# Kernel optimization log

Hardware: AMD Instinct MI355X
Metric: run time of the kernel (lower is better)

Reference implementation:

```python
import jax, jax.numpy as jnp
import numpy as np

FLT_BACKWARP = 2.5  # Matching.fltBackwarp for intLevel == 4
NEG_SLOPE = 0.1


def backwarp(ten_input, ten_flow):
    # torch grid_sample(mode='bilinear', padding_mode='zeros', align_corners=True)
    # with grid = base + flow*2/(size-1) is equivalent to sampling at pixel coords
    # (x + u, y + v) with zero padding outside [0, W-1] x [0, H-1].
    B, C, H, W = ten_input.shape
    xs = jnp.arange(W, dtype=ten_input.dtype)
    ys = jnp.arange(H, dtype=ten_input.dtype)
    px = xs[None, None, :] + ten_flow[:, 0]  # [B,H,W]
    py = ys[None, :, None] + ten_flow[:, 1]  # [B,H,W]
    x0 = jnp.floor(px)
    y0 = jnp.floor(py)
    x1 = x0 + 1.0
    y1 = y0 + 1.0
    wx1 = px - x0
    wx0 = 1.0 - wx1
    wy1 = py - y0
    wy0 = 1.0 - wy1

    def gather(ix, iy):
        valid = ((ix >= 0) & (ix <= W - 1) & (iy >= 0) & (iy <= H - 1)).astype(ten_input.dtype)
        ixc = jnp.clip(ix, 0, W - 1).astype(jnp.int32)
        iyc = jnp.clip(iy, 0, H - 1).astype(jnp.int32)
        v = jax.vmap(lambda img, yy, xx: img[:, yy, xx])(ten_input, iyc, ixc)  # [B,C,H,W]
        return v * valid[:, None]

    return (gather(x0, y0) * (wx0 * wy0)[:, None]
            + gather(x1, y0) * (wx1 * wy0)[:, None]
            + gather(x0, y1) * (wx0 * wy1)[:, None]
            + gather(x1, y1) * (wx1 * wy1)[:, None])


def correlation(one, two, stride):
    # FunctionCorrelation: 7x7 displacement window, offsets (-3..3)*stride,
    # zero pad 3*stride, dot over channels / C. Output [B,49,ceil(H/s),ceil(W/s)].
    B, C, H, W = one.shape
    p = 3 * stride
    two_pad = jnp.pad(two, ((0, 0), (0, 0), (p, p), (p, p)))
    one_s = one[:, :, ::stride, ::stride]  # [B,C,Ho,Wo]
    outs = []
    for dj in range(-3, 4):  # channel index k = (dj+3)*7 + (di+3)
        for di in range(-3, 4):
            y0 = p + dj * stride
            x0 = p + di * stride
            shift = two_pad[:, :, y0:y0 + H:stride, x0:x0 + W:stride]
            outs.append(jnp.einsum('bchw,bchw->bhw', one_s, shift))
    return jnp.stack(outs, axis=1) / jnp.asarray(C, one.dtype)


def setup_inputs() -> dict:
    key = jax.random.key(0)
    k1, k2, k3 = jax.random.split(key, 3)
    B, C, H, W = 2, 128, 256, 448
    return {
        'tenOne': jax.random.normal(k1, (B, C, H, W), dtype=jnp.float32),
        'tenTwo': jax.random.normal(k2, (B, C, H, W), dtype=jnp.float32),
        'tenFlow': jax.random.normal(k3, (B, 2, H, W), dtype=jnp.float32),
        'intStride': 1,
    }


def reference(tenOne, tenTwo, tenFlow, intStride):
    warped = backwarp(tenTwo, tenFlow * FLT_BACKWARP)
    corr = correlation(tenOne, warped, int(intStride))
    return jax.nn.leaky_relu(corr, NEG_SLOPE)
```

## Files before the change

### kernel.cpp

```cpp
#include <hip/hip_runtime.h>
#include <hip/hip_bf16.h>

#define BB 2
#define CC 128
#define HH 256
#define WW 448
#define KK 49
#define HWSZ (HH * WW)
#define PW 456

#define WT_BYTES ((size_t)BB * HH * PW * CC * 2)
#define TWT_BYTES ((size_t)BB * HH * WW * CC * 2)
#define WS_NEED (WT_BYTES + TWT_BYTES)

typedef __attribute__((ext_vector_type(8))) short bf16x8;
typedef __attribute__((ext_vector_type(4))) float f32x4;
typedef __attribute__((ext_vector_type(8))) unsigned short u16x8;

static __device__ __forceinline__ short f2bf(float v) {
  __hip_bfloat16 h = __float2bfloat16(v);
  return *reinterpret_cast<short*>(&h);
}
static __device__ __forceinline__ float bf2f(unsigned short u) {
  unsigned int x = ((unsigned int)u) << 16;
  return __uint_as_float(x);
}

__global__ __launch_bounds__(256) void border_kernel(__hip_bfloat16* wt) {
  int i = blockIdx.x * 256 + threadIdx.x;
  int by = i >> 7;
  int r = i & 127;
  int ps = r >> 4;
  int c16 = r & 15;
  int px = (ps < 4) ? ps : (448 + ps);
  u16x8 z = {0, 0, 0, 0, 0, 0, 0, 0};
  *(u16x8*)((char*)wt + ((size_t)((size_t)by * PW + px) * CC + c16 * 8) * 2) = z;
}

__global__ __launch_bounds__(256) void transpose_kernel(
    const float* __restrict__ two, __hip_bfloat16* __restrict__ two_t) {
  __shared__ float lds[128 * 33];
  int bid = blockIdx.x;
  int b = bid / (HWSZ / 32);
  int tile = bid - b * (HWSZ / 32);
  int P0 = tile * 32;

  const float* src = two + (size_t)b * CC * HWSZ + P0;
  int t = threadIdx.x;
  int bc = t >> 3;
  int f = t & 7;
#pragma unroll
  for (int k = 0; k < 4; ++k) {
    int c = bc + k * 32;
    float4 v = *(const float4*)(src + (size_t)c * HWSZ + f * 4);
    float* d = &lds[c * 33 + f * 4];
    d[0] = v.x; d[1] = v.y; d[2] = v.z; d[3] = v.w;
  }
  __syncthreads();

  int q = t & 7;
  int pl = t >> 3;
  int cs = q * 16;
  u16x8 pk0, pk1;
#pragma unroll
  for (int j = 0; j < 8; ++j)
    pk0[j] = (unsigned short)f2bf(lds[(cs + j) * 33 + pl]);
#pragma unroll
  for (int j = 0; j < 8; ++j)
    pk1[j] = (unsigned short)f2bf(lds[(cs + 8 + j) * 33 + pl]);
  char* dst = (char*)two_t + ((size_t)((size_t)b * HWSZ + P0 + pl) * CC + cs) * 2;
  *(u16x8*)dst = pk0;
  *(u16x8*)(dst + 16) = pk1;
}

__global__ __launch_bounds__(256) void warp_fast(
    const __hip_bfloat16* __restrict__ two_t, const float* __restrict__ flow,
    __hip_bfloat16* __restrict__ wt) {
  int wg = (blockIdx.x & 7) * 128 + (blockIdx.x >> 3);
  int b = wg >> 9;
  int rem = wg & 511;
  int y = rem >> 1;
  int X0 = (rem & 1) * 224;
  int pg = threadIdx.x >> 4;
  int cw = threadIdx.x & 15;

  const char* tb = (const char*)two_t + (size_t)b * HWSZ * (CC * 2);
  char* wb = (char*)wt + ((size_t)(b * HH + y) * PW + 4) * (CC * 2);
  const float* fxp = flow + (size_t)(b * 2 + 0) * HWSZ + y * WW;
  const float* fyp = flow + (size_t)(b * 2 + 1) * HWSZ + y * WW;

#pragma unroll 2
  for (int it = 0; it < 14; ++it) {
    int x = X0 + it * 16 + pg;

    float fx = fxp[x] * 2.5f;
    float fy = fyp[x] * 2.5f;
    float px = (float)x + fx;
    float py = (float)y + fy;
    float x0f = floorf(px), y0f = floorf(py);
    int x0 = (int)x0f, y0 = (int)y0f;
    int x1 = x0 + 1, y1 = y0 + 1;
    float wx1 = px - x0f, wx0 = 1.0f - wx1;
    float wy1 = py - y0f, wy0 = 1.0f - wy1;
    bool vx0 = (x0 >= 0) && (x0 < WW);
    bool vx1 = (x1 >= 0) && (x1 < WW);
    bool vy0 = (y0 >= 0) && (y0 < HH);
    bool vy1 = (y1 >= 0) && (y1 < HH);
    float w00 = (vx0 && vy0) ? wx0 * wy0 : 0.0f;
    float w01 = (vx1 && vy0) ? wx1 * wy0 : 0.0f;
    float w10 = (vx0 && vy1) ? wx0 * wy1 : 0.0f;
    float w11 = (vx1 && vy1) ? wx1 * wy1 : 0.0f;
    int cx0 = min(max(x0, 0), WW - 1);
    int cx1 = min(max(x1, 0), WW - 1);
    int cy0 = min(max(y0, 0), HH - 1);
    int cy1 = min(max(y1, 0), HH - 1);

    u16x8 a = *(const u16x8*)(tb + ((size_t)cy0 * WW + cx0) * 256 + cw * 16);
    u16x8 bb_ = *(const u16x8*)(tb + ((size_t)cy0 * WW + cx1) * 256 + cw * 16);
    u16x8 c = *(const u16x8*)(tb + ((size_t)cy1 * WW + cx0) * 256 + cw * 16);
    u16x8 d = *(const u16x8*)(tb + ((size_t)cy1 * WW + cx1) * 256 + cw * 16);

    u16x8 pk;
#pragma unroll
    for (int e = 0; e < 8; ++e) {
      float v = w00 * bf2f((unsigned short)a[e]) +
                w01 * bf2f((unsigned short)bb_[e]) +
                w10 * bf2f((unsigned short)c[e]) +
                w11 * bf2f((unsigned short)d[e]);
      pk[e] = (unsigned short)f2bf(v);
    }
    *(u16x8*)(wb + (size_t)x * 256 + cw * 16) = pk;
  }
}

__global__ __launch_bounds__(256) void warp_fallback(
    const float* __restrict__ two, const float* __restrict__ flow,
    __hip_bfloat16* __restrict__ wt) {
  int idx = blockIdx.x * 256 + threadIdx.x;
  if (idx >= BB * HWSZ) return;
  int x = idx % WW;
  int y = (idx / WW) % HH;
  int b = idx / HWSZ;

  float fx = flow[(b * 2 + 0) * HWSZ + y * WW + x] * 2.5f;
  float fy = flow[(b * 2 + 1) * HWSZ + y * WW + x] * 2.5f;
  float px = (float)x + fx;
  float py = (float)y + fy;
  float x0f = floorf(px), y0f = floorf(py);
  int x0 = (int)x0f, y0 = (int)y0f;
  int x1 = x0 + 1, y1 = y0 + 1;
  float wx1 = px - x0f, wx0 = 1.0f - wx1;
  float wy1 = py - y0f, wy0 = 1.0f - wy1;
  bool vx0 = (x0 >= 0) && (x0 < WW);
  bool vx1 = (x1 >= 0) && (x1 < WW);
  bool vy0 = (y0 >= 0) && (y0 < HH);
  bool vy1 = (y1 >= 0) && (y1 < HH);
  float w00 = (vx0 && vy0) ? wx0 * wy0 : 0.0f;
  float w01 = (vx1 && vy0) ? wx1 * wy0 : 0.0f;
  float w10 = (vx0 && vy1) ? wx0 * wy1 : 0.0f;
  float w11 = (vx1 && vy1) ? wx1 * wy1 : 0.0f;
  int cx0 = min(max(x0, 0), WW - 1);
  int cx1 = min(max(x1, 0), WW - 1);
  int cy0 = min(max(y0, 0), HH - 1);
  int cy1 = min(max(y1, 0), HH - 1);
  int o00 = cy0 * WW + cx0;
  int o01 = cy0 * WW + cx1;
  int o10 = cy1 * WW + cx0;
  int o11 = cy1 * WW + cx1;

  const float* p = two + (size_t)b * CC * HWSZ;
  char* wo = (char*)wt + ((size_t)((size_t)(b * HH + y) * PW) + x + 4) * CC * 2;
#pragma unroll 4
  for (int j = 0; j < 16; ++j) {
    u16x8 pk;
#pragma unroll
    for (int jj = 0; jj < 8; ++jj) {
      int c = j * 8 + jj;
      const float* pc = p + (size_t)c * HWSZ;
      float v = w00 * pc[o00] + w01 * pc[o01] + w10 * pc[o10] + w11 * pc[o11];
      pk[jj] = (unsigned short)f2bf(v);
    }
    *(u16x8*)(wo + j * 16) = pk;
  }
}

#define YTB 8
#define NROWS 14
#define NPOS 22
#define ROWCH (NPOS * 16)
#define CHUNKS (NROWS * ROWCH)

__global__ __launch_bounds__(512) void corr_kernel(
    const float* __restrict__ one, const __hip_bfloat16* __restrict__ wt,
    float* __restrict__ out) {
  __shared__ uint4 ldsb[CHUNKS];

  int bid = blockIdx.x;
  int wg = (bid & 7) * 224 + (bid >> 3);
  int b = wg / 896;
  int rem = wg - b * 896;
  int xt = rem >> 5;
  int yt = rem & 31;
  int ybase = yt * YTB;
  int X0 = xt * 16;
  int tid = threadIdx.x;

  const char* wbase =
      (const char*)wt + (((size_t)(b * HH)) * PW + X0 + 1) * (CC * 2);
#pragma unroll
  for (int k = 0; k < 10; ++k) {
    int ci = tid + k * 512;
    if (ci < CHUNKS) {
      int row = ci / ROWCH;
      int r2 = ci - row * ROWCH;
      int p = r2 >> 4;
      int cw = r2 & 15;
      int yy = ybase - 3 + row;
      uint4 v = {0, 0, 0, 0};
      if (yy >= 0 && yy < HH)
        v = *(const uint4*)(wbase + (size_t)yy * (PW * CC * 2) + p * 256 +
                            cw * 16);
      *(uint4*)((char*)ldsb + ((ci * 16) ^ ((p & 7) << 4))) = v;
    }
  }
  __syncthreads();

  int w = tid >> 6;
  int l = tid & 63;
  int lp = l & 15;
  int lg = l >> 4;
  int y = ybase + w;

  const float* Abase = one + ((size_t)(b * CC) * HH + y) * WW + X0 + lp;
  int p1 = (lp + 16 < 21) ? (lp + 16) : 21;
  int sw0 = (lp & 7) << 4;
  int sw1 = (p1 & 7) << 4;

  f32x4 acc[7][2] = {};

#pragma unroll
  for (int t = 0; t < 4; ++t) {
    bf16x8 a;
#pragma unroll
    for (int j = 0; j < 8; ++j)
      a[j] = f2bf(Abase[(size_t)(t * 32 + lg * 8 + j) * HWSZ]);
    int co = t * 64 + lg * 16;
#pragma unroll
    for (int dj = 0; dj < 7; ++dj) {
      int rl = w + dj;
      int a0 = (((rl * NPOS + lp) << 8) + co) ^ sw0;
      int a1 = (((rl * NPOS + p1) << 8) + co) ^ sw1;
      bf16x8 b0 = *(const bf16x8*)((const char*)ldsb + a0);
      bf16x8 b1 = *(const bf16x8*)((const char*)ldsb + a1);
      acc[dj][0] =
          __builtin_amdgcn_mfma_f32_16x16x32_bf16(a, b0, acc[dj][0], 0, 0, 0);
      acc[dj][1] =
          __builtin_amdgcn_mfma_f32_16x16x32_bf16(a, b1, acc[dj][1], 0, 0, 0);
    }
  }

  __syncthreads();
  float* sc = (float*)ldsb;
#pragma unroll
  for (int dj = 0; dj < 7; ++dj) {
#pragma unroll
    for (int nt = 0; nt < 2; ++nt) {
      int post = lp + 16 * nt;
#pragma unroll
      for (int r = 0; r < 4; ++r) {
        int xlc = 4 * lg + r;
        int di = post - xlc;
        if (di >= 0 && di <= 6) {
          int k = dj * 7 + di;
          sc[k * 128 + w * 16 + ((xlc + k) & 15)] = acc[dj][nt][r];
        }
      }
    }
  }
  __syncthreads();

  float* ob = out + (size_t)(b * KK) * HWSZ + (size_t)ybase * WW + X0;
#pragma unroll
  for (int i = 0; i < 13; ++i) {
    int e = tid + i * 512;
    if (e < KK * 128) {
      int k = e >> 7;
      int yr = (e >> 4) & 7;
      int px = e & 15;
      float v = sc[k * 128 + yr * 16 + ((px + k) & 15)] * (1.0f / 128.0f);
      v = (v > 0.0f) ? v : 0.1f * v;
      ob[(size_t)k * HWSZ + yr * WW + px] = v;
    }
  }
}

extern "C" void kernel_launch(void* const* d_in, const int* in_sizes, int n_in,
                              void* d_out, int out_size, void* d_ws,
                              size_t ws_size, hipStream_t stream) {
  const float* tenOne = (const float*)d_in[0];
  const float* tenTwo = (const float*)d_in[1];
  const float* tenFlow = (const float*)d_in[2];

  __hip_bfloat16* wt = (__hip_bfloat16*)d_ws;
  border_kernel<<<256, 256, 0, stream>>>(wt);

  if (ws_size >= WS_NEED) {
    __hip_bfloat16* two_t = (__hip_bfloat16*)((char*)d_ws + WT_BYTES);
    transpose_kernel<<<BB * (HWSZ / 32), 256, 0, stream>>>(tenTwo, two_t);
    warp_fast<<<1024, 256, 0, stream>>>(two_t, tenFlow, wt);
  } else {
    int blocks = (BB * HWSZ + 255) / 256;
    warp_fallback<<<blocks, 256, 0, stream>>>(tenTwo, tenFlow, wt);
  }
  corr_kernel<<<1792, 512, 0, stream>>>(tenOne, wt, (float*)d_out);
}
```

Measured before the change: 134.1 us.

## Overlap LDS staging loads with A-operand loads and reorder MFMA loop

The correlation kernel now issues all global loads for the warped-feature tile into registers, then loads and converts the full A operand (tenOne channels) before writing the staged data into LDS. Both sets of global-memory latency are overlapped instead of being serialized behind a barrier. The MFMA loop is reordered so the displacement row is outermost and the A fragments are preloaded, and launch bounds now request 4 blocks per SM. The cost is much higher register pressure (10 uint4 plus 32 floats held live), which can cause spills or fail to meet the occupancy hint.

```diff
diff --git a/kernel.cpp b/kernel.cpp
--- a/kernel.cpp
+++ b/kernel.cpp
@@ -190,7 +190,7 @@
 #define ROWCH (NPOS * 16)
 #define CHUNKS (NROWS * ROWCH)
 
-__global__ __launch_bounds__(512) void corr_kernel(
+__global__ __launch_bounds__(512, 4) void corr_kernel(
     const float* __restrict__ one, const __hip_bfloat16* __restrict__ wt,
     float* __restrict__ out) {
   __shared__ uint4 ldsb[CHUNKS];
@@ -205,57 +205,73 @@
   int X0 = xt * 16;
   int tid = threadIdx.x;
 
-  const char* wbase =
-      (const char*)wt + (((size_t)(b * HH)) * PW + X0 + 1) * (CC * 2);
-#pragma unroll
-  for (int k = 0; k < 10; ++k) {
-    int ci = tid + k * 512;
-    if (ci < CHUNKS) {
-      int row = ci / ROWCH;
-      int r2 = ci - row * ROWCH;
-      int p = r2 >> 4;
-      int cw = r2 & 15;
-      int yy = ybase - 3 + row;
-      uint4 v = {0, 0, 0, 0};
-      if (yy >= 0 && yy < HH)
-        v = *(const uint4*)(wbase + (size_t)yy * (PW * CC * 2) + p * 256 +
-                            cw * 16);
-      *(uint4*)((char*)ldsb + ((ci * 16) ^ ((p & 7) << 4))) = v;
-    }
-  }
-  __syncthreads();
-
   int w = tid >> 6;
   int l = tid & 63;
   int lp = l & 15;
   int lg = l >> 4;
   int y = ybase + w;
 
+  const char* wbase =
+      (const char*)wt + (((size_t)(b * HH)) * PW + X0 + 1) * (CC * 2);
+  uint4 sv[10];
+  int lofs[10];
+#pragma unroll
+  for (int k = 0; k < 10; ++k) {
+    int ci = tid + k * 512;
+    int row = ci / ROWCH;
+    int r2 = ci - row * ROWCH;
+    int p = r2 >> 4;
+    int cw = r2 & 15;
+    int yy = ybase - 3 + row;
+    uint4 v = {0, 0, 0, 0};
+    if (ci < CHUNKS && yy >= 0 && yy < HH)
+      v = *(const uint4*)(wbase + (size_t)yy * (PW * CC * 2) + p * 256 +
+                          cw * 16);
+    sv[k] = v;
+    lofs[k] = (ci * 16) ^ ((p & 7) << 4);
+  }
+
   const float* Abase = one + ((size_t)(b * CC) * HH + y) * WW + X0 + lp;
+  float af[32];
+#pragma unroll
+  for (int t = 0; t < 4; ++t)
+#pragma unroll
+    for (int j = 0; j < 8; ++j)
+      af[t * 8 + j] = Abase[(size_t)(t * 32 + lg * 8 + j) * HWSZ];
+  bf16x8 afr[4];
+#pragma unroll
+  for (int t = 0; t < 4; ++t)
+#pragma unroll
+    for (int j = 0; j < 8; ++j) afr[t][j] = f2bf(af[t * 8 + j]);
+
+#pragma unroll
+  for (int k = 0; k < 10; ++k)
+    if (tid + k * 512 < CHUNKS) *(uint4*)((char*)ldsb + lofs[k]) = sv[k];
+  __syncthreads();
+
   int p1 = (lp + 16 < 21) ? (lp + 16) : 21;
-  int sw0 = (lp & 7) << 4;
-  int sw1 = (p1 & 7) << 4;
+  int cosw0[4], cosw1[4];
+#pragma unroll
+  for (int t = 0; t < 4; ++t) {
+    int co = t * 64 + lg * 16;
+    cosw0[t] = co ^ ((lp & 7) << 4);
+    cosw1[t] = co ^ ((p1 & 7) << 4);
+  }
 
   f32x4 acc[7][2] = {};
-
-#pragma unroll
-  for (int t = 0; t < 4; ++t) {
-    bf16x8 a;
-#pragma unroll
-    for (int j = 0; j < 8; ++j)
-      a[j] = f2bf(Abase[(size_t)(t * 32 + lg * 8 + j) * HWSZ]);
-    int co = t * 64 + lg * 16;
-#pragma unroll
-    for (int dj = 0; dj < 7; ++dj) {
-      int rl = w + dj;
-      int a0 = (((rl * NPOS + lp) << 8) + co) ^ sw0;
-      int a1 = (((rl * NPOS + p1) << 8) + co) ^ sw1;
-      bf16x8 b0 = *(const bf16x8*)((const char*)ldsb + a0);
-      bf16x8 b1 = *(const bf16x8*)((const char*)ldsb + a1);
+#pragma unroll
+  for (int dj = 0; dj < 7; ++dj) {
+    int rl = w + dj;
+    int b0 = (rl * NPOS + lp) << 8;
+    int b1 = (rl * NPOS + p1) << 8;
+#pragma unroll
+    for (int t = 0; t < 4; ++t) {
+      bf16x8 v0 = *(const bf16x8*)((const char*)ldsb + (b0 + cosw0[t]));
+      bf16x8 v1 = *(const bf16x8*)((const char*)ldsb + (b1 + cosw1[t]));
       acc[dj][0] =
-          __builtin_amdgcn_mfma_f32_16x16x32_bf16(a, b0, acc[dj][0], 0, 0, 0);
+          __builtin_amdgcn_mfma_f32_16x16x32_bf16(afr[t], v0, acc[dj][0], 0, 0, 0);
       acc[dj][1] =
-          __builtin_amdgcn_mfma_f32_16x16x32_bf16(a, b1, acc[dj][1], 0, 0, 0);
+          __builtin_amdgcn_mfma_f32_16x16x32_bf16(afr[t], v1, acc[dj][1], 0, 0, 0);
     }
   }
 
```

Result: no change. 134.0 us (-0.0%).

## Shrink correlation tile to 4 rows and stage warped channels in two halves

Applied to the files above, without the earlier changes.

The correlation kernel now uses 256-thread blocks covering 4 output rows instead of 8, which doubles the grid. The warped-feature halo is loaded into LDS in two 64-channel halves, so the LDS footprint is roughly a third of before. The bf16 A fragments from tenOne are prefetched into registers before the first LDS fill to overlap global loads. The smaller footprint is meant to raise occupancy, at the cost of more halo re-reads (10 rows per 4 outputs instead of 14 per 8) and an extra barrier per block.

```diff
diff --git a/kernel.cpp b/kernel.cpp
--- a/kernel.cpp
+++ b/kernel.cpp
@@ -184,46 +184,26 @@
   }
 }
 
-#define YTB 8
-#define NROWS 14
+#define YTB 4
+#define NROWS 10
 #define NPOS 22
-#define ROWCH (NPOS * 16)
-#define CHUNKS (NROWS * ROWCH)
-
-__global__ __launch_bounds__(512) void corr_kernel(
+#define HROWCH (NPOS * 8)
+#define HCHUNKS (NROWS * HROWCH)
+
+__global__ __launch_bounds__(256) void corr_kernel(
     const float* __restrict__ one, const __hip_bfloat16* __restrict__ wt,
     float* __restrict__ out) {
-  __shared__ uint4 ldsb[CHUNKS];
+  __shared__ uint4 ldsb[HCHUNKS];
 
   int bid = blockIdx.x;
-  int wg = (bid & 7) * 224 + (bid >> 3);
-  int b = wg / 896;
-  int rem = wg - b * 896;
-  int xt = rem >> 5;
-  int yt = rem & 31;
+  int wg = (bid & 7) * 448 + (bid >> 3);
+  int b = wg / 1792;
+  int rem = wg - b * 1792;
+  int xt = rem >> 6;
+  int yt = rem & 63;
   int ybase = yt * YTB;
   int X0 = xt * 16;
   int tid = threadIdx.x;
-
-  const char* wbase =
-      (const char*)wt + (((size_t)(b * HH)) * PW + X0 + 1) * (CC * 2);
-#pragma unroll
-  for (int k = 0; k < 10; ++k) {
-    int ci = tid + k * 512;
-    if (ci < CHUNKS) {
-      int row = ci / ROWCH;
-      int r2 = ci - row * ROWCH;
-      int p = r2 >> 4;
-      int cw = r2 & 15;
-      int yy = ybase - 3 + row;
-      uint4 v = {0, 0, 0, 0};
-      if (yy >= 0 && yy < HH)
-        v = *(const uint4*)(wbase + (size_t)yy * (PW * CC * 2) + p * 256 +
-                            cw * 16);
-      *(uint4*)((char*)ldsb + ((ci * 16) ^ ((p & 7) << 4))) = v;
-    }
-  }
-  __syncthreads();
 
   int w = tid >> 6;
   int l = tid & 63;
@@ -232,6 +212,16 @@
   int y = ybase + w;
 
   const float* Abase = one + ((size_t)(b * CC) * HH + y) * WW + X0 + lp;
+  bf16x8 afr[4];
+#pragma unroll
+  for (int t = 0; t < 4; ++t) {
+#pragma unroll
+    for (int j = 0; j < 8; ++j)
+      afr[t][j] = f2bf(Abase[(size_t)(t * 32 + lg * 8 + j) * HWSZ]);
+  }
+
+  const char* wbase =
+      (const char*)wt + (((size_t)(b * HH)) * PW + X0 + 1) * (CC * 2);
   int p1 = (lp + 16 < 21) ? (lp + 16) : 21;
   int sw0 = (lp & 7) << 4;
   int sw1 = (p1 & 7) << 4;
@@ -239,23 +229,41 @@
   f32x4 acc[7][2] = {};
 
 #pragma unroll
-  for (int t = 0; t < 4; ++t) {
-    bf16x8 a;
-#pragma unroll
-    for (int j = 0; j < 8; ++j)
-      a[j] = f2bf(Abase[(size_t)(t * 32 + lg * 8 + j) * HWSZ]);
-    int co = t * 64 + lg * 16;
+  for (int h = 0; h < 2; ++h) {
+    if (h) __syncthreads();
+#pragma unroll
+    for (int k = 0; k < 7; ++k) {
+      int ci = tid + k * 256;
+      if (ci < HCHUNKS) {
+        int row = ci / HROWCH;
+        int r2 = ci - row * HROWCH;
+        int p = r2 >> 3;
+        int cw = r2 & 7;
+        int yy = ybase - 3 + row;
+        uint4 v = {0, 0, 0, 0};
+        if (yy >= 0 && yy < HH)
+          v = *(const uint4*)(wbase + (size_t)yy * (PW * CC * 2) + p * 256 +
+                              h * 128 + cw * 16);
+        *(uint4*)((char*)ldsb + ((ci * 16) ^ ((p & 7) << 4))) = v;
+      }
+    }
+    __syncthreads();
+
 #pragma unroll
     for (int dj = 0; dj < 7; ++dj) {
       int rl = w + dj;
-      int a0 = (((rl * NPOS + lp) << 8) + co) ^ sw0;
-      int a1 = (((rl * NPOS + p1) << 8) + co) ^ sw1;
-      bf16x8 b0 = *(const bf16x8*)((const char*)ldsb + a0);
-      bf16x8 b1 = *(const bf16x8*)((const char*)ldsb + a1);
-      acc[dj][0] =
-          __builtin_amdgcn_mfma_f32_16x16x32_bf16(a, b0, acc[dj][0], 0, 0, 0);
-      acc[dj][1] =
-          __builtin_amdgcn_mfma_f32_16x16x32_bf16(a, b1, acc[dj][1], 0, 0, 0);
+      int b0 = (rl * NPOS + lp) << 7;
+      int b1 = (rl * NPOS + p1) << 7;
+#pragma unroll
+      for (int tl = 0; tl < 2; ++tl) {
+        int co = tl * 64 + lg * 16;
+        bf16x8 v0 = *(const bf16x8*)((const char*)ldsb + (b0 + (co ^ sw0)));
+        bf16x8 v1 = *(const bf16x8*)((const char*)ldsb + (b1 + (co ^ sw1)));
+        acc[dj][0] = __builtin_amdgcn_mfma_f32_16x16x32_bf16(
+            afr[h * 2 + tl], v0, acc[dj][0], 0, 0, 0);
+        acc[dj][1] = __builtin_amdgcn_mfma_f32_16x16x32_bf16(
+            afr[h * 2 + tl], v1, acc[dj][1], 0, 0, 0);
+      }
     }
   }
 
@@ -272,7 +280,7 @@
         int di = post - xlc;
         if (di >= 0 && di <= 6) {
           int k = dj * 7 + di;
-          sc[k * 128 + w * 16 + ((xlc + k) & 15)] = acc[dj][nt][r];
+          sc[k * 64 + w * 16 + ((xlc + k) & 15)] = acc[dj][nt][r];
         }
       }
     }
@@ -282,12 +290,12 @@
   float* ob = out + (size_t)(b * KK) * HWSZ + (size_t)ybase * WW + X0;
 #pragma unroll
   for (int i = 0; i < 13; ++i) {
-    int e = tid + i * 512;
-    if (e < KK * 128) {
-      int k = e >> 7;
-      int yr = (e >> 4) & 7;
+    int e = tid + i * 256;
+    if (e < KK * 64) {
+      int k = e >> 6;
+      int yr = (e >> 4) & 3;
       int px = e & 15;
-      float v = sc[k * 128 + yr * 16 + ((px + k) & 15)] * (1.0f / 128.0f);
+      float v = sc[k * 64 + yr * 16 + ((px + k) & 15)] * (1.0f / 128.0f);
       v = (v > 0.0f) ? v : 0.1f * v;
       ob[(size_t)k * HWSZ + yr * WW + px] = v;
     }
@@ -312,5 +320,5 @@
     int blocks = (BB * HWSZ + 255) / 256;
     warp_fallback<<<blocks, 256, 0, stream>>>(tenTwo, tenFlow, wt);
   }
-  corr_kernel<<<1792, 512, 0, stream>>>(tenOne, wt, (float*)d_out);
-}
+  corr_kernel<<<3584, 256, 0, stream>>>(tenOne, wt, (float*)d_out);
+}
```

Result: slower. 154.7 us (+15.4%).
